# Kernel tuning notes

Hardware: AMD Instinct MI355X
Metric: run time of the kernel (lower is better)

Reference implementation:

```python
import jax, jax.numpy as jnp
import numpy as np

N, M, D = 131072, 2048, 2


def setup_inputs() -> dict:
    key = jax.random.key(0)
    k1, k2 = jax.random.split(key)
    sample = jax.random.normal(k1, (N, D), dtype=jnp.float32)
    mu = jax.random.uniform(k2, (M, D), dtype=jnp.float32)
    # A initialized as 15 * I per component, exactly as in the torch module
    A = (15.0 * jnp.broadcast_to(jnp.eye(D, dtype=jnp.float32), (M, D, D))).astype(jnp.float32)
    w = jnp.ones((M, 1), dtype=jnp.float32)
    return {"sample": sample, "mu": mu, "A": A, "w": w}


def reference(sample, mu, A, w):
    """GaussianMixture.log_likelihoods(sample): logsumexp_j( wlog_j - (x-mu_j)^T G_j (x-mu_j) )."""
    # update_covariances: G_m = A_m A_m^T / 2, shape (M, D, D)
    G = jnp.einsum('mij,mkj->mik', A, A) * 0.5
    g00, g01, g10, g11 = G[:, 0, 0], G[:, 0, 1], G[:, 1, 0], G[:, 1, 1]  # (M,)
    # covariances_determinants (2x2 case) + weights_log
    dets = g00 * g11 - g01 * g10                                          # (M,)
    wlog = jax.nn.log_softmax(w, axis=0)[:, 0] + 0.5 * jnp.log(dets)      # (M,)
    # Pairwise Mahalanobis quadratic form, D=2 expanded to avoid an (N,M,D) temp
    dx0 = sample[:, 0:1] - mu[None, :, 0]   # (N, M)
    dx1 = sample[:, 1:2] - mu[None, :, 1]   # (N, M)
    q = g00 * dx0 * dx0 + (g01 + g10) * dx0 * dx1 + g11 * dx1 * dx1       # (N, M)
    # mode='lse' reduction of kernel_product: log sum_j exp(wlog_j - q_ij)
    ll = jax.nn.logsumexp(wlog[None, :] - q, axis=1, keepdims=True)       # (N, 1)
    return ll
```

## Files before the change

kernel.cpp:

```cpp
#include <hip/hip_runtime.h>
#include <math.h>


#if __has_builtin(__builtin_amdgcn_exp2f)
#define EXP2(x) __builtin_amdgcn_exp2f(x)
#else
#define EXP2(x) exp2f(x)
#endif

typedef float v2f   __attribute__((ext_vector_type(2)));
typedef float f32x4 __attribute__((ext_vector_type(4)));
typedef short bf16x8 __attribute__((ext_vector_type(8)));
typedef float v4f __attribute__((ext_vector_type(4)));
typedef int   i4v __attribute__((ext_vector_type(4)));

#if __has_builtin(__builtin_elementwise_max)
#define VMAX(a, b) __builtin_elementwise_max(a, b)
#else
static __device__ inline v2f VMAX(v2f a, v2f b) {
  v2f r; r.x = fmaxf(a.x, b.x); r.y = fmaxf(a.y, b.y); return r;
}
static __device__ inline v4f VMAX(v4f a, v4f b) {
  v4f r; r.x = fmaxf(a.x, b.x); r.y = fmaxf(a.y, b.y);
  r.z = fmaxf(a.z, b.z); r.w = fmaxf(a.w, b.w); return r;
}
#endif

#define SCH_K1   8388608.0f
#define SCH_K2   1064986823.0f
#define SCH_TMIN 58353856.0f

#define SPLIT 8
#define CH  16
#define RMF 8
#define LOG2E 1.44269504088896340736f
#define LN2   0.69314718055994530942f

__device__ __forceinline__ unsigned short f2bf(float f) {
  unsigned u = __builtin_bit_cast(unsigned, f);
  unsigned r = u + 0x7FFFu + ((u >> 16) & 1u);
  return (unsigned short)(r >> 16);
}
__device__ __forceinline__ float bf2f(unsigned short h) {
  unsigned u = ((unsigned)h) << 16;
  return __builtin_bit_cast(float, u);
}

__global__ __launch_bounds__(256) void prep_kernel(
    const float* __restrict__ mu,
    const float* __restrict__ A,
    const float* __restrict__ w,
    float* __restrict__ C,
    int M) {
  __shared__ float red[256];
  __shared__ int uni[256];
  const int t = threadIdx.x;

  float mx = -INFINITY;
  for (int m = t; m < M; m += 256) mx = fmaxf(mx, w[m]);
  red[t] = mx; __syncthreads();
  for (int s = 128; s > 0; s >>= 1) {
    if (t < s) red[t] = fmaxf(red[t], red[t + s]);
    __syncthreads();
  }
  const float wmax = red[0]; __syncthreads();

  float sum = 0.f;
  for (int m = t; m < M; m += 256) sum += expf(w[m] - wmax);
  red[t] = sum; __syncthreads();
  for (int s = 128; s > 0; s >>= 1) {
    if (t < s) red[t] += red[t + s];
    __syncthreads();
  }
  const float logZ = wmax + logf(red[0]);

  const float r00 = A[0], r01 = A[1], r10 = A[2], r11 = A[3];
  const float rg00 = 0.5f * (r00 * r00 + r01 * r01);
  const float rg01 = 0.5f * (r00 * r10 + r01 * r11);
  const float rg11 = 0.5f * (r10 * r10 + r11 * r11);

  unsigned short* Bp = (unsigned short*)(C + 6 * M + 16);

  int myuni = 1;
  for (int m = t; m < M; m += 256) {
    const float a00 = A[m * 4 + 0], a01 = A[m * 4 + 1];
    const float a10 = A[m * 4 + 2], a11 = A[m * 4 + 3];
    const float g00 = 0.5f * (a00 * a00 + a01 * a01);
    const float g01 = 0.5f * (a00 * a10 + a01 * a11);
    const float g11 = 0.5f * (a10 * a10 + a11 * a11);
    const float g01s = 2.0f * g01;
    const float det = g00 * g11 - g01 * g01;
    const float wlog = (w[m] - logZ) + 0.5f * logf(det);
    const float mu0 = mu[m * 2 + 0], mu1 = mu[m * 2 + 1];
    const float c0 = wlog - (g00 * mu0 * mu0 + g01s * mu0 * mu1 + g11 * mu1 * mu1);
    const float c2 = 2.0f * g00 * mu0 + g01s * mu1;
    const float c4 = 2.0f * g11 * mu1 + g01s * mu0;
    const float C0v = LOG2E * c0;
    const float C2v = LOG2E * c2;
    const float C4v = LOG2E * c4;
    C[0 * M + m] = C0v;
    C[1 * M + m] = LOG2E * -g00;
    C[2 * M + m] = C2v;
    C[3 * M + m] = LOG2E * -g11;
    C[4 * M + m] = C4v;
    C[5 * M + m] = LOG2E * -g01s;
    const unsigned short c2h = f2bf(C2v);
    const unsigned short c2l = f2bf(C2v - bf2f(c2h));
    const unsigned short c4h = f2bf(C4v);
    const unsigned short c4l = f2bf(C4v - bf2f(c4h));
    const unsigned short c0h = f2bf(C0v);
    const unsigned short c0l = f2bf(C0v - bf2f(c0h));
    Bp[m * 8 + 0] = c2h; Bp[m * 8 + 1] = c2h; Bp[m * 8 + 2] = c2l;
    Bp[m * 8 + 3] = c4h; Bp[m * 8 + 4] = c4h; Bp[m * 8 + 5] = c4l;
    Bp[m * 8 + 6] = c0h; Bp[m * 8 + 7] = c0l;
    myuni &= (g00 == rg00) & (g01 == rg01) & (g11 == rg11);
  }
  uni[t] = myuni; __syncthreads();
  for (int s = 128; s > 0; s >>= 1) {
    if (t < s) uni[t] &= uni[t + s];
    __syncthreads();
  }
  if (t == 0) {
    ((int*)C)[6 * M + 0] = uni[0];
    C[6 * M + 1] = LOG2E * -rg00;
    C[6 * M + 2] = LOG2E * -rg11;
    C[6 * M + 3] = LOG2E * -2.0f * rg01;
  }
}

#define EPI(J, MXJ, SJ) do {                                                 \
    const float a0 = acc[0][J], a1 = acc[1][J], a2 = acc[2][J],              \
                a3 = acc[3][J], a4 = acc[4][J], a5 = acc[5][J],              \
                a6 = acc[6][J], a7 = acc[7][J];                              \
    const float m01 = fmaxf(a0, a1), m23 = fmaxf(a2, a3);                    \
    const float m45 = fmaxf(a4, a5), m67 = fmaxf(a6, a7);                    \
    const float cm = fmaxf(fmaxf(m01, m23), fmaxf(m45, m67));                \
    const float nm = fmaxf(MXJ, cm);                                         \
    const float resc = EXP2(MXJ - nm);                                       \
    const float knm = fmaf(nm, -SCH_K1, SCH_K2);                             \
    const float e0 = __builtin_bit_cast(float, (int)fmaxf(fmaf(a0, SCH_K1, knm), SCH_TMIN)); \
    const float e1 = __builtin_bit_cast(float, (int)fmaxf(fmaf(a1, SCH_K1, knm), SCH_TMIN)); \
    const float e2 = __builtin_bit_cast(float, (int)fmaxf(fmaf(a2, SCH_K1, knm), SCH_TMIN)); \
    const float e3 = __builtin_bit_cast(float, (int)fmaxf(fmaf(a3, SCH_K1, knm), SCH_TMIN)); \
    const float e4 = __builtin_bit_cast(float, (int)fmaxf(fmaf(a4, SCH_K1, knm), SCH_TMIN)); \
    const float e5 = __builtin_bit_cast(float, (int)fmaxf(fmaf(a5, SCH_K1, knm), SCH_TMIN)); \
    const float e6 = __builtin_bit_cast(float, (int)fmaxf(fmaf(a6, SCH_K1, knm), SCH_TMIN)); \
    const float e7 = __builtin_bit_cast(float, (int)fmaxf(fmaf(a7, SCH_K1, knm), SCH_TMIN)); \
    const float sm = ((e0 + e1) + (e2 + e3)) + ((e4 + e5) + (e6 + e7));      \
    SJ = fmaf(SJ, resc, sm);                                                 \
    MXJ = nm;                                                                \
  } while (0)

#define MERGE(MXJ, SJ, OFF) do {                                             \
    const float om = __shfl_xor(MXJ, OFF, 64);                               \
    const float os = __shfl_xor(SJ, OFF, 64);                                \
    const float nm = fmaxf(MXJ, om);                                         \
    SJ = SJ * EXP2(MXJ - nm) + os * EXP2(om - nm);                           \
    MXJ = nm;                                                                \
  } while (0)

__global__ __launch_bounds__(512, 3) void gmix_mfma(
    const float2* __restrict__ xs,
    const float* __restrict__ C,
    float* __restrict__ out,
    int N, int M) {
  __shared__ float Lmx[SPLIT][2][64];
  __shared__ float Lsm[SPLIT][2][64];
  const int lane = threadIdx.x & 63;
  const int wave = __builtin_amdgcn_readfirstlane((int)(threadIdx.x >> 6));
  const int flag = ((const int*)C)[6 * M + 0];
  const float cb1 = C[6 * M + 1];
  const float cb3 = C[6 * M + 2];
  const float cb5 = C[6 * M + 3];

  if (flag) {
    const bf16x8* __restrict__ Bv = (const bf16x8*)(C + 6 * M + 16);
    const int sbase = blockIdx.x * 128 + wave * 16;
    const int col = lane & 15;

    const int sA = sbase + col;
    const float2 xa = (sA < N) ? xs[sA] : make_float2(0.f, 0.f);
    bf16x8 afrag = (bf16x8){0, 0, 0, 0, 0, 0, 0, 0};
    if (lane < 16) {
      const unsigned short x0h = f2bf(xa.x);
      const unsigned short x0l = f2bf(xa.x - bf2f(x0h));
      const unsigned short x1h = f2bf(xa.y);
      const unsigned short x1l = f2bf(xa.y - bf2f(x1h));
      afrag = (bf16x8){(short)x0h, (short)x0l, (short)x0h,
                       (short)x1h, (short)x1l, (short)x1h,
                       (short)0x3F80, (short)0x3F80};
    }

    float mx0 = -INFINITY, mx1 = -INFINITY, mx2 = -INFINITY, mx3 = -INFINITY;
    float s0 = 0.f, s1 = 0.f, s2 = 0.f, s3 = 0.f;
    const f32x4 z4 = {0.f, 0.f, 0.f, 0.f};
    const int rounds = M / (RMF * 16);

#pragma unroll 2
    for (int t = 0; t < rounds; ++t) {
      f32x4 acc[RMF];
#pragma unroll
      for (int r = 0; r < RMF; ++r) {
        const bf16x8 bfrag = Bv[t * (RMF * 16) + r * 16 + col];
        acc[r] = __builtin_amdgcn_mfma_f32_16x16x32_bf16(afrag, bfrag, z4, 0, 0, 0);
      }
      EPI(0, mx0, s0);
      EPI(1, mx1, s1);
      EPI(2, mx2, s2);
      EPI(3, mx3, s3);
    }

#pragma unroll
    for (int off = 1; off < 16; off <<= 1) {
      MERGE(mx0, s0, off);
      MERGE(mx1, s1, off);
      MERGE(mx2, s2, off);
      MERGE(mx3, s3, off);
    }

    if (col == 0) {
      const int g = lane >> 4;
#define OUTJ(J, MXJ, SJ) do {                                                \
        const int sr = sbase + g * 4 + (J);                                  \
        if (sr < N) {                                                        \
          const float2 xo = xs[sr];                                          \
          const float base = cb1 * xo.x * xo.x + cb3 * xo.y * xo.y +         \
                             cb5 * xo.x * xo.y;                              \
          out[sr] = (MXJ + base + __log2f(SJ)) * LN2;                        \
        }                                                                    \
      } while (0)
      OUTJ(0, mx0, s0);
      OUTJ(1, mx1, s1);
      OUTJ(2, mx2, s2);
      OUTJ(3, mx3, s3);
#undef OUTJ
    }
  } else {
    const int nA = blockIdx.x * 128 + lane;
    const int nB = nA + 64;
    const float2 xA = (nA < N) ? xs[nA] : make_float2(0.f, 0.f);
    const float2 xB = (nB < N) ? xs[nB] : make_float2(0.f, 0.f);
    const v2f x0p = {xA.x, xB.x};
    const v2f x1p = {xA.y, xB.y};

    const int Mq = M / SPLIT;
    const int m0 = wave * Mq;
    const float* __restrict__ C0 = C + m0;
    const float* __restrict__ C1 = C + M + m0;
    const float* __restrict__ C2 = C + 2 * M + m0;
    const float* __restrict__ C3 = C + 3 * M + m0;
    const float* __restrict__ C4 = C + 4 * M + m0;
    const float* __restrict__ C5 = C + 5 * M + m0;

    v2f mx = {-INFINITY, -INFINITY};
    v2f sacc = {0.f, 0.f};
    for (int m = 0; m < Mq; m += CH) {
      v2f a[CH];
#pragma unroll
      for (int j = 0; j < CH; ++j) {
        const float c0 = C0[m + j], c1 = C1[m + j], c2 = C2[m + j];
        const float c3 = C3[m + j], c4 = C4[m + j], c5 = C5[m + j];
        v2f u = x0p * c1 + c2;
        u = x1p * c5 + u;
        v2f v = x1p * c3 + c4;
        v2f r = u * x0p + c0;
        a[j] = v * x1p + r;
      }
      v2f t0 = VMAX(a[0], a[1]);
      v2f t1 = VMAX(a[2], a[3]);
      v2f t2 = VMAX(a[4], a[5]);
      v2f t3 = VMAX(a[6], a[7]);
#pragma unroll
      for (int j = 8; j < CH; j += 4) {
        t0 = VMAX(t0, a[j]);     t1 = VMAX(t1, a[j + 1]);
        t2 = VMAX(t2, a[j + 2]); t3 = VMAX(t3, a[j + 3]);
      }
      const v2f cm = VMAX(VMAX(t0, t1), VMAX(t2, t3));
      const v2f nm = VMAX(mx, cm);
      v2f resc; resc.x = EXP2(mx.x - nm.x); resc.y = EXP2(mx.y - nm.y);
      v2f l0 = {0.f, 0.f}, l1 = {0.f, 0.f};
#pragma unroll
      for (int j = 0; j < CH; j += 2) {
        const v2f d0 = a[j] - nm, d1 = a[j + 1] - nm;
        v2f e0, e1;
        e0.x = EXP2(d0.x); e0.y = EXP2(d0.y);
        e1.x = EXP2(d1.x); e1.y = EXP2(d1.y);
        l0 += e0; l1 += e1;
      }
      sacc = sacc * resc + (l0 + l1);
      mx = nm;
    }
    const v2f base = cb1 * x0p * x0p + cb3 * x1p * x1p + cb5 * x0p * x1p;
#pragma unroll
    for (int k = 0; k < 2; ++k) {
      Lmx[wave][k][lane] = mx[k] + base[k];
      Lsm[wave][k][lane] = sacc[k];
    }
    __syncthreads();
    if (wave < 2) {
      const int n = blockIdx.x * 128 + wave * 64 + lane;
      if (n < N) {
        float gm = Lmx[0][wave][lane];
#pragma unroll
        for (int v = 1; v < SPLIT; ++v) gm = fmaxf(gm, Lmx[v][wave][lane]);
        float S = 0.f;
#pragma unroll
        for (int v = 0; v < SPLIT; ++v)
          S += Lsm[v][wave][lane] * EXP2(Lmx[v][wave][lane] - gm);
        out[n] = (gm + __log2f(S)) * LN2;
      }
    }
  }
}

__global__ __launch_bounds__(512, 4) void gmix_kernel(
    const float* __restrict__ sample,
    const float* __restrict__ C,
    float* __restrict__ out,
    int N, int M) {
  __shared__ float Lmx[SPLIT][4][64];
  __shared__ float Lsm[SPLIT][4][64];

  const int lane = threadIdx.x & 63;
  const int wave = __builtin_amdgcn_readfirstlane((int)(threadIdx.x >> 6));
  const int n0 = blockIdx.x * 256 + lane;

  float2 xs0 = (n0       < N) ? ((const float2*)sample)[n0      ] : make_float2(0.f, 0.f);
  float2 xs1 = (n0 + 64  < N) ? ((const float2*)sample)[n0 + 64 ] : make_float2(0.f, 0.f);
  float2 xs2 = (n0 + 128 < N) ? ((const float2*)sample)[n0 + 128] : make_float2(0.f, 0.f);
  float2 xs3 = (n0 + 192 < N) ? ((const float2*)sample)[n0 + 192] : make_float2(0.f, 0.f);
  const v4f x0q = {xs0.x, xs1.x, xs2.x, xs3.x};
  const v4f x1q = {xs0.y, xs1.y, xs2.y, xs3.y};

  const int flag = ((const int*)C)[6 * M + 0];
  const float cb1 = C[6 * M + 1];
  const float cb3 = C[6 * M + 2];
  const float cb5 = C[6 * M + 3];

  const int Mq = M / SPLIT;
  const int m0 = wave * Mq;
  const float* __restrict__ C0 = C + m0;
  const float* __restrict__ C1 = C + M + m0;
  const float* __restrict__ C2 = C + 2 * M + m0;
  const float* __restrict__ C3 = C + 3 * M + m0;
  const float* __restrict__ C4 = C + 4 * M + m0;
  const float* __restrict__ C5 = C + 5 * M + m0;

  v4f base4 = {0.f, 0.f, 0.f, 0.f};
  v4f mx = {-INFINITY, -INFINITY, -INFINITY, -INFINITY};
  v4f s  = {0.f, 0.f, 0.f, 0.f};
  const v4f tminv4 = {SCH_TMIN, SCH_TMIN, SCH_TMIN, SCH_TMIN};

  if (flag) {
    base4 = cb1 * x0q * x0q + cb3 * x1q * x1q + cb5 * x0q * x1q;
    for (int m = 0; m < Mq; m += CH) {
      v4f a[CH];
#pragma unroll
      for (int j = 0; j < CH; ++j) {
        const float c0 = C0[m + j], c2 = C2[m + j], c4 = C4[m + j];
        v4f t = x0q * c2 + c0;
        a[j] = x1q * c4 + t;
      }
      v4f t0 = VMAX(a[0], a[1]);
      v4f t1 = VMAX(a[2], a[3]);
      v4f t2 = VMAX(a[4], a[5]);
      v4f t3 = VMAX(a[6], a[7]);
#pragma unroll
      for (int j = 8; j < CH; j += 4) {
        t0 = VMAX(t0, a[j]);     t1 = VMAX(t1, a[j + 1]);
        t2 = VMAX(t2, a[j + 2]); t3 = VMAX(t3, a[j + 3]);
      }
      const v4f cm = VMAX(VMAX(t0, t1), VMAX(t2, t3));
      const v4f nm = VMAX(mx, cm);
      v4f resc;
      resc.x = EXP2(mx.x - nm.x); resc.y = EXP2(mx.y - nm.y);
      resc.z = EXP2(mx.z - nm.z); resc.w = EXP2(mx.w - nm.w);
      const v4f knm = SCH_K2 - nm * SCH_K1;
      v4f l0 = {0.f, 0.f, 0.f, 0.f}, l1 = {0.f, 0.f, 0.f, 0.f};
#pragma unroll
      for (int j = 0; j < CH; j += 2) {
        v4f u0 = a[j]     * SCH_K1 + knm;
        v4f u1 = a[j + 1] * SCH_K1 + knm;
        u0 = VMAX(u0, tminv4);
        u1 = VMAX(u1, tminv4);
        const i4v iv0 = __builtin_convertvector(u0, i4v);
        const i4v iv1 = __builtin_convertvector(u1, i4v);
        l0 += __builtin_bit_cast(v4f, iv0);
        l1 += __builtin_bit_cast(v4f, iv1);
      }
      s = s * resc + (l0 + l1);
      mx = nm;
    }
  } else {
    for (int m = 0; m < Mq; m += CH) {
      v4f a[CH];
#pragma unroll
      for (int j = 0; j < CH; ++j) {
        const float c0 = C0[m + j], c1 = C1[m + j], c2 = C2[m + j];
        const float c3 = C3[m + j], c4 = C4[m + j], c5 = C5[m + j];
        v4f u = x0q * c1 + c2;
        u = x1q * c5 + u;
        v4f v = x1q * c3 + c4;
        v4f r = u * x0q + c0;
        a[j] = v * x1q + r;
      }
      v4f t0 = VMAX(a[0], a[1]);
      v4f t1 = VMAX(a[2], a[3]);
      v4f t2 = VMAX(a[4], a[5]);
      v4f t3 = VMAX(a[6], a[7]);
#pragma unroll
      for (int j = 8; j < CH; j += 4) {
        t0 = VMAX(t0, a[j]);     t1 = VMAX(t1, a[j + 1]);
        t2 = VMAX(t2, a[j + 2]); t3 = VMAX(t3, a[j + 3]);
      }
      const v4f cm = VMAX(VMAX(t0, t1), VMAX(t2, t3));
      const v4f nm = VMAX(mx, cm);
      v4f resc;
      resc.x = EXP2(mx.x - nm.x); resc.y = EXP2(mx.y - nm.y);
      resc.z = EXP2(mx.z - nm.z); resc.w = EXP2(mx.w - nm.w);
      v4f l0 = {0.f, 0.f, 0.f, 0.f}, l1 = {0.f, 0.f, 0.f, 0.f};
#pragma unroll
      for (int j = 0; j < CH; j += 2) {
        v4f d0 = a[j] - nm, d1 = a[j + 1] - nm;
        v4f e0, e1;
        e0.x = EXP2(d0.x); e0.y = EXP2(d0.y); e0.z = EXP2(d0.z); e0.w = EXP2(d0.w);
        e1.x = EXP2(d1.x); e1.y = EXP2(d1.y); e1.z = EXP2(d1.z); e1.w = EXP2(d1.w);
        l0 += e0; l1 += e1;
      }
      s = s * resc + (l0 + l1);
      mx = nm;
    }
  }

#pragma unroll
  for (int k = 0; k < 4; ++k) {
    Lmx[wave][k][lane] = mx[k] + base4[k];
    Lsm[wave][k][lane] = s[k];
  }
  __syncthreads();

  if (wave < 4) {
    const int set = wave;
    const int n = blockIdx.x * 256 + set * 64 + lane;
    if (n < N) {
      float gm = Lmx[0][set][lane];
#pragma unroll
      for (int v = 1; v < SPLIT; ++v) gm = fmaxf(gm, Lmx[v][set][lane]);
      float S = 0.f;
#pragma unroll
      for (int v = 0; v < SPLIT; ++v)
        S += Lsm[v][set][lane] * EXP2(Lmx[v][set][lane] - gm);
      out[n] = (gm + __log2f(S)) * LN2;
    }
  }
}

extern "C" void kernel_launch(void* const* d_in, const int* in_sizes, int n_in,
                              void* d_out, int out_size, void* d_ws, size_t ws_size,
                              hipStream_t stream) {
  const float* sample = (const float*)d_in[0];
  const float* mu     = (const float*)d_in[1];
  const float* A      = (const float*)d_in[2];
  const float* w      = (const float*)d_in[3];
  float* out = (float*)d_out;

  const int N = in_sizes[0] / 2;
  const int M = in_sizes[3];

  float* C = (float*)d_ws;
  const size_t need = ((size_t)6 * M + 16) * 4 + (size_t)M * 16;

  prep_kernel<<<1, 256, 0, stream>>>(mu, A, w, C, M);

  if (ws_size >= need && M % (RMF * 16) == 0 && M % (SPLIT * CH) == 0) {
    gmix_mfma<<<(N + 127) / 128, 512, 0, stream>>>(
        (const float2*)sample, C, out, N, M);
  } else {
    gmix_kernel<<<(N + 255) / 256, 512, 0, stream>>>(sample, C, out, N, M);
  }
}
```

Measured before the change: 114.7 us.

## Use lazy max rescaling with threshold and unsigned-convert Schraudolph exp

```diff
diff --git a/kernel.cpp b/kernel.cpp
--- a/kernel.cpp
+++ b/kernel.cpp
@@ -32,7 +32,8 @@
 
 #define SPLIT 8
 #define CH  16
-#define RMF 8
+#define RMF 4
+#define THR 40.0f
 #define LOG2E 1.44269504088896340736f
 #define LN2   0.69314718055994530942f
 
@@ -44,6 +45,13 @@
 __device__ __forceinline__ float bf2f(unsigned short h) {
   unsigned u = ((unsigned)h) << 16;
   return __builtin_bit_cast(float, u);
+}
+
+__device__ __forceinline__ float sch_e(float a, float knm) {
+  const float u = fmaf(a, SCH_K1, knm);
+  unsigned r;
+  asm("v_cvt_u32_f32 %0, %1" : "=v"(r) : "v"(u));
+  return __builtin_bit_cast(float, r);
 }
 
 __global__ __launch_bounds__(256) void prep_kernel(
@@ -128,29 +136,6 @@
   }
 }
 
-#define EPI(J, MXJ, SJ) do {                                                 \
-    const float a0 = acc[0][J], a1 = acc[1][J], a2 = acc[2][J],              \
-                a3 = acc[3][J], a4 = acc[4][J], a5 = acc[5][J],              \
-                a6 = acc[6][J], a7 = acc[7][J];                              \
-    const float m01 = fmaxf(a0, a1), m23 = fmaxf(a2, a3);                    \
-    const float m45 = fmaxf(a4, a5), m67 = fmaxf(a6, a7);                    \
-    const float cm = fmaxf(fmaxf(m01, m23), fmaxf(m45, m67));                \
-    const float nm = fmaxf(MXJ, cm);                                         \
-    const float resc = EXP2(MXJ - nm);                                       \
-    const float knm = fmaf(nm, -SCH_K1, SCH_K2);                             \
-    const float e0 = __builtin_bit_cast(float, (int)fmaxf(fmaf(a0, SCH_K1, knm), SCH_TMIN)); \
-    const float e1 = __builtin_bit_cast(float, (int)fmaxf(fmaf(a1, SCH_K1, knm), SCH_TMIN)); \
-    const float e2 = __builtin_bit_cast(float, (int)fmaxf(fmaf(a2, SCH_K1, knm), SCH_TMIN)); \
-    const float e3 = __builtin_bit_cast(float, (int)fmaxf(fmaf(a3, SCH_K1, knm), SCH_TMIN)); \
-    const float e4 = __builtin_bit_cast(float, (int)fmaxf(fmaf(a4, SCH_K1, knm), SCH_TMIN)); \
-    const float e5 = __builtin_bit_cast(float, (int)fmaxf(fmaf(a5, SCH_K1, knm), SCH_TMIN)); \
-    const float e6 = __builtin_bit_cast(float, (int)fmaxf(fmaf(a6, SCH_K1, knm), SCH_TMIN)); \
-    const float e7 = __builtin_bit_cast(float, (int)fmaxf(fmaf(a7, SCH_K1, knm), SCH_TMIN)); \
-    const float sm = ((e0 + e1) + (e2 + e3)) + ((e4 + e5) + (e6 + e7));      \
-    SJ = fmaf(SJ, resc, sm);                                                 \
-    MXJ = nm;                                                                \
-  } while (0)
-
 #define MERGE(MXJ, SJ, OFF) do {                                             \
     const float om = __shfl_xor(MXJ, OFF, 64);                               \
     const float os = __shfl_xor(SJ, OFF, 64);                                \
@@ -159,7 +144,7 @@
     MXJ = nm;                                                                \
   } while (0)
 
-__global__ __launch_bounds__(512, 3) void gmix_mfma(
+__global__ __launch_bounds__(512, 8) void gmix_mfma(
     const float2* __restrict__ xs,
     const float* __restrict__ C,
     float* __restrict__ out,
@@ -174,9 +159,9 @@
   const float cb5 = C[6 * M + 3];
 
   if (flag) {
-    const bf16x8* __restrict__ Bv = (const bf16x8*)(C + 6 * M + 16);
     const int sbase = blockIdx.x * 128 + wave * 16;
     const int col = lane & 15;
+    const bf16x8* __restrict__ Bcol = (const bf16x8*)(C + 6 * M + 16) + col;
 
     const int sA = sbase + col;
     const float2 xa = (sA < N) ? xs[sA] : make_float2(0.f, 0.f);
@@ -193,21 +178,42 @@
 
     float mx0 = -INFINITY, mx1 = -INFINITY, mx2 = -INFINITY, mx3 = -INFINITY;
     float s0 = 0.f, s1 = 0.f, s2 = 0.f, s3 = 0.f;
+    float knm0 = 0.f, knm1 = 0.f, knm2 = 0.f, knm3 = 0.f;
     const f32x4 z4 = {0.f, 0.f, 0.f, 0.f};
     const int rounds = M / (RMF * 16);
 
-#pragma unroll 2
     for (int t = 0; t < rounds; ++t) {
       f32x4 acc[RMF];
 #pragma unroll
       for (int r = 0; r < RMF; ++r) {
-        const bf16x8 bfrag = Bv[t * (RMF * 16) + r * 16 + col];
+        const bf16x8 bfrag = Bcol[t * (RMF * 16) + r * 16];
         acc[r] = __builtin_amdgcn_mfma_f32_16x16x32_bf16(afrag, bfrag, z4, 0, 0, 0);
       }
-      EPI(0, mx0, s0);
-      EPI(1, mx1, s1);
-      EPI(2, mx2, s2);
-      EPI(3, mx3, s3);
+      const float cm0 = fmaxf(fmaxf(fmaxf(acc[0][0], acc[1][0]), acc[2][0]), acc[3][0]);
+      const float cm1 = fmaxf(fmaxf(fmaxf(acc[0][1], acc[1][1]), acc[2][1]), acc[3][1]);
+      const float cm2 = fmaxf(fmaxf(fmaxf(acc[0][2], acc[1][2]), acc[2][2]), acc[3][2]);
+      const float cm3 = fmaxf(fmaxf(fmaxf(acc[0][3], acc[1][3]), acc[2][3]), acc[3][3]);
+      const float d = fmaxf(fmaxf(cm0 - mx0, cm1 - mx1),
+                            fmaxf(cm2 - mx2, cm3 - mx3));
+      if (__any(d > THR)) {
+#define RESC(J) do {                                                         \
+          const float nm_ = fmaxf(mx##J, cm##J);                             \
+          s##J *= EXP2(mx##J - nm_);                                         \
+          mx##J = nm_;                                                       \
+          knm##J = fmaf(nm_, -SCH_K1, SCH_K2);                               \
+        } while (0)
+        RESC(0); RESC(1); RESC(2); RESC(3);
+#undef RESC
+      }
+#define EPIC(J) do {                                                         \
+        const float e0 = sch_e(acc[0][J], knm##J);                           \
+        const float e1 = sch_e(acc[1][J], knm##J);                           \
+        const float e2 = sch_e(acc[2][J], knm##J);                           \
+        const float e3 = sch_e(acc[3][J], knm##J);                           \
+        s##J += (e0 + e1) + (e2 + e3);                                       \
+      } while (0)
+      EPIC(0); EPIC(1); EPIC(2); EPIC(3);
+#undef EPIC
     }
 
 #pragma unroll
```

Result: faster. 111.8 us (-2.5%).
